# Performance work log

Hardware: AMD Instinct MI355X
Metric: run time of the kernel (lower is better)

The kernel has to match this reference:

```python
import jax, jax.numpy as jnp
import numpy as np

V, E_DIM, HID, GNN_O, HEADS = 50257, 256, 128, 128, 4
N_NODES, N_EDGES, T_LEN = 10000, 160000, 64
NEG_SLOPE = 0.2


def gatv2(x, src, dst, Wl, Wr, att, bias, concat):
    """PyG GATv2Conv (share_weights=False, self-loops already in src/dst)."""
    heads, out_ch = att.shape
    n = x.shape[0]
    xl = (x @ Wl).reshape(n, heads, out_ch)   # source transform
    xr = (x @ Wr).reshape(n, heads, out_ch)   # target transform
    e = jax.nn.leaky_relu(xl[src] + xr[dst], NEG_SLOPE)        # [E, h, c]
    logits = jnp.einsum('ehc,hc->eh', e, att)                  # [E, h]
    m = jax.ops.segment_max(logits, dst, num_segments=n)
    a = jnp.exp(logits - m[dst])
    a = a / jax.ops.segment_sum(a, dst, num_segments=n)[dst]
    out = jax.ops.segment_sum(xl[src] * a[..., None], dst, num_segments=n)
    out = out.reshape(n, heads * out_ch) if concat else out.mean(axis=1)
    return out + bias


def setup_inputs() -> dict:
    key = jax.random.key(0)
    ks = jax.random.split(key, 16)
    g = lambda k, shape: jax.random.normal(k, shape, jnp.float32) * 0.05
    x_nodes = jax.random.randint(ks[0], (N_NODES,), 0, V)
    edge_index = jax.random.randint(ks[1], (2, N_EDGES), 0, N_NODES)
    target_sequence = jax.random.randint(ks[2], (1, T_LEN), 0, V)
    return dict(
        x_nodes=x_nodes, edge_index=edge_index, target_sequence=target_sequence,
        embedding=g(ks[3], (V, E_DIM)),
        W1l=g(ks[4], (E_DIM, HEADS * HID)), W1r=g(ks[5], (E_DIM, HEADS * HID)),
        att1=g(ks[6], (HEADS, HID)), b1=jnp.zeros((HEADS * HID,), jnp.float32),
        W2l=g(ks[7], (HEADS * HID, GNN_O)), W2r=g(ks[8], (HEADS * HID, GNN_O)),
        att2=g(ks[9], (1, GNN_O)), b2=jnp.zeros((GNN_O,), jnp.float32),
        Wih=g(ks[10], (3 * HID, GNN_O + E_DIM)), Whh=g(ks[11], (3 * HID, HID)),
        bih=jnp.zeros((3 * HID,), jnp.float32), bhh=jnp.zeros((3 * HID,), jnp.float32),
        Wout=g(ks[12], (V, HID)), bout=jnp.zeros((V,), jnp.float32),
    )


def reference(x_nodes, edge_index, target_sequence, embedding,
              W1l, W1r, att1, b1, W2l, W2r, att2, b2,
              Wih, Whh, bih, bhh, Wout, bout):
    n = x_nodes.shape[0]
    loops = jnp.arange(n, dtype=edge_index.dtype)
    src = jnp.concatenate([edge_index[0], loops])   # add self-loops (PyG default)
    dst = jnp.concatenate([edge_index[1], loops])
    feats = embedding[x_nodes]                      # [N, E_DIM] (dropout off: eval)
    h1 = jax.nn.elu(gatv2(feats, src, dst, W1l, W1r, att1, b1, concat=True))
    enc = gatv2(h1, src, dst, W2l, W2r, att2, b2, concat=False)  # [N, GNN_O]
    context = enc.mean(axis=0)                      # constant across decode steps

    # teacher forcing (ratio=1.0): input tokens are SOS(0) then shifted targets
    tokens = jnp.concatenate([jnp.zeros((1,), target_sequence.dtype),
                              target_sequence[0, :-1]])

    def step(h, tok):
        x = jnp.concatenate([embedding[tok], context])          # [E_DIM+GNN_O]
        gi = Wih @ x + bih
        gh = Whh @ h + bhh
        ir, iz, inn = jnp.split(gi, 3)
        hr, hz, hn = jnp.split(gh, 3)
        r = jax.nn.sigmoid(ir + hr)
        z = jax.nn.sigmoid(iz + hz)
        cand = jnp.tanh(inn + r * hn)
        h_new = (1.0 - z) * cand + z * h
        logits = Wout @ h_new + bout
        return h_new, logits

    h0 = jnp.zeros((Whh.shape[1],), jnp.float32)
    _, logits = jax.lax.scan(step, h0, tokens)      # [T, V]
    return logits[None]                              # [1, T, V]
```

## Files before the change

### kernel.cpp

```cpp
#include <hip/hip_runtime.h>
#include <hip/hip_bf16.h>
#include <math.h>

#define NNODES 10000
#define NEDGES 160000
#define EDIM   256
#define HIDC   128
#define TLEN   64
#define VOCAB  50257
#define NEG    0.2f
#define NCTXSLOT 32

typedef __bf16 bf16x8 __attribute__((ext_vector_type(8)));
typedef float  f32x4  __attribute__((ext_vector_type(4)));

static __device__ __forceinline__ float leaky(float x){ return x > 0.f ? x : NEG*x; }
static __device__ __forceinline__ float sigm (float x){ return __fdividef(1.f, 1.f + __expf(-x)); }
static __device__ __forceinline__ float eluf (float x){ return x > 0.f ? x : expm1f(x); }
static __device__ __forceinline__ unsigned short bf16rn(float f){
  unsigned a = __float_as_uint(f);
  return (unsigned short)((a + 0x7FFFu + ((a >> 16) & 1u)) >> 16);
}
static __device__ __forceinline__ float upf(unsigned short u){ return __uint_as_float(((unsigned)u) << 16); }
static __device__ __forceinline__ float4 up4(ushort4 u){
  float4 f; f.x = upf(u.x); f.y = upf(u.y); f.z = upf(u.z); f.w = upf(u.w); return f;
}
static __device__ __forceinline__ unsigned char fp8e4m3(float f){
  return (unsigned char)(__builtin_amdgcn_cvt_pk_fp8_f32(f, f, 0, false) & 0xFF);
}
static __device__ __forceinline__ float4 up8x4(unsigned d){
  auto lo = __builtin_amdgcn_cvt_pk_f32_fp8((int)d, false);
  auto hi = __builtin_amdgcn_cvt_pk_f32_fp8((int)d, true);
  float4 f; f.x = lo[0]; f.y = lo[1]; f.z = hi[0]; f.w = hi[1]; return f;
}

#define PB_FEATS 2500
#define PB_WCAST 8783
#define PB_TR1L  8815
#define PB_TR1R  8847
#define PB_TR2L  8863
#define PB_TR2R  8879
#define PB_ZERO  8919
#define PB_AT    9047

static __device__ void tr_dev(const float* __restrict__ in, unsigned short* __restrict__ out,
                              int K, int Nin, int bx, int by, int t,
                              unsigned short (*tile)[72])
{
  int k0 = bx*64, n0 = by*64;
  int tr = t >> 4, tc4 = (t & 15)*4;
  #pragma unroll
  for (int it = 0; it < 4; ++it){
    int kr = tr + 16*it;
    float4 v = *(const float4*)(in + (size_t)(k0+kr)*Nin + n0 + tc4);
    tile[tc4+0][kr] = bf16rn(v.x);
    tile[tc4+1][kr] = bf16rn(v.y);
    tile[tc4+2][kr] = bf16rn(v.z);
    tile[tc4+3][kr] = bf16rn(v.w);
  }
  __syncthreads();
  #pragma unroll
  for (int it = 0; it < 4; ++it){
    int nr = tr + 16*it;
    ushort4 o;
    o.x = tile[nr][tc4+0]; o.y = tile[nr][tc4+1];
    o.z = tile[nr][tc4+2]; o.w = tile[nr][tc4+3];
    *(ushort4*)(out + (size_t)(n0+nr)*K + k0 + tc4) = o;
  }
}

__global__ __launch_bounds__(256) void k_prep(
    const int* __restrict__ xn, const float* __restrict__ emb,
    unsigned short* __restrict__ featsb,
    const float* __restrict__ Wout, unsigned short* __restrict__ Woutb,
    const float* __restrict__ W1l, const float* __restrict__ W1r, unsigned short* __restrict__ Bt1,
    const float* __restrict__ W2l, const float* __restrict__ W2r, unsigned short* __restrict__ Bt2,
    int* __restrict__ deg, int* __restrict__ cursor, float* __restrict__ ctxp,
    const int* __restrict__ tseq, const float* __restrict__ Wih,
    const float* __restrict__ bih, float* __restrict__ At)
{
  __shared__ unsigned short tile[64][72];
  __shared__ __align__(16) float xe[EDIM];
  int b = blockIdx.x, t = threadIdx.x;
  if (b < PB_FEATS){
    int node = b*4 + (t >> 6);
    int l = t & 63;
    float4 v = ((const float4*)(emb + (size_t)xn[node]*EDIM))[l];
    ushort4 o; o.x = bf16rn(v.x); o.y = bf16rn(v.y); o.z = bf16rn(v.z); o.w = bf16rn(v.w);
    *(ushort4*)(featsb + (size_t)node*EDIM + 4*l) = o;
  } else if (b < PB_WCAST){
    int idx = (b - PB_FEATS)*256 + t;
    if (idx < VOCAB*HIDC/4){
      float4 v = ((const float4*)Wout)[idx];
      ushort4 o; o.x = bf16rn(v.x); o.y = bf16rn(v.y); o.z = bf16rn(v.z); o.w = bf16rn(v.w);
      ((ushort4*)Woutb)[idx] = o;
    }
  } else if (b < PB_TR1L){
    int lb = b - PB_WCAST;  tr_dev(W1l, Bt1,           256, 512, lb & 3, lb >> 2, t, tile);
  } else if (b < PB_TR1R){
    int lb = b - PB_TR1L;   tr_dev(W1r, Bt1 + 512*256, 256, 512, lb & 3, lb >> 2, t, tile);
  } else if (b < PB_TR2L){
    int lb = b - PB_TR1R;   tr_dev(W2l, Bt2,           512, 128, lb & 7, lb >> 3, t, tile);
  } else if (b < PB_TR2R){
    int lb = b - PB_TR2L;   tr_dev(W2r, Bt2 + 128*512, 512, 128, lb & 7, lb >> 3, t, tile);
  } else if (b < PB_ZERO){
    int gid = (b - PB_TR2R)*256 + t;
    if (gid < NNODES){ deg[gid] = 0; cursor[gid] = 0; }
    if (gid < NCTXSLOT*HIDC) ctxp[gid] = 0.f;
  } else {
    int lb = b - PB_ZERO;
    int tt = lb >> 1;
    int row = (lb & 1)*192 + t;
    int tok = (tt == 0) ? 0 : tseq[tt-1];
    {
      if (t < 64) ((float4*)xe)[t] = ((const float4*)(emb + (size_t)tok*EDIM))[t];
      __syncthreads();
    }
    if (t < 192){
      const float4* w4 = (const float4*)(Wih + (size_t)row*384);
      const float4* x4 = (const float4*)xe;
      float a0 = 0.f, a1 = 0.f, a2 = 0.f, a3 = 0.f;
      #pragma unroll
      for (int k = 0; k < 64; k++){
        float4 w = w4[k]; float4 x = x4[k];
        a0 = fmaf(w.x, x.x, a0); a1 = fmaf(w.y, x.y, a1);
        a2 = fmaf(w.z, x.z, a2); a3 = fmaf(w.w, x.w, a3);
      }
      At[tt*384 + row] = ((a0 + a1) + (a2 + a3)) + bih[row];
    }
  }
}

__global__ void k_deg(const int* __restrict__ dst, int* __restrict__ deg){
  int e = blockIdx.x*256 + threadIdx.x;
  if (e < NEDGES) atomicAdd(&deg[dst[e]], 1);
}

__global__ __launch_bounds__(1024) void k_scan(const int* __restrict__ deg, int* __restrict__ offs){
  __shared__ int s[1024];
  int t = threadIdx.x;
  int loc[10]; int sum = 0;
  #pragma unroll
  for (int q = 0; q < 10; q++){
    int idx = t*10 + q;
    loc[q] = sum;
    sum += (idx < NNODES) ? deg[idx] : 0;
  }
  s[t] = sum;
  __syncthreads();
  for (int ofs = 1; ofs < 1024; ofs <<= 1){
    int v = (t >= ofs) ? s[t-ofs] : 0;
    __syncthreads();
    s[t] += v;
    __syncthreads();
  }
  int pre = (t > 0) ? s[t-1] : 0;
  #pragma unroll
  for (int q = 0; q < 10; q++){
    int idx = t*10 + q;
    if (idx < NNODES) offs[idx] = pre + loc[q];
  }
  if (t == 1023) offs[NNODES] = s[1023];
}

__global__ void k_scatter(const int* __restrict__ src, const int* __restrict__ dst,
                          const int* __restrict__ offs, int* __restrict__ cursor,
                          int* __restrict__ esrc){
  int e = blockIdx.x*256 + threadIdx.x;
  if (e >= NEDGES) return;
  int d = dst[e];
  int p = atomicAdd(&cursor[d], 1);
  esrc[offs[d] + p] = src[e];
}

template<int KDIM>
__global__ __launch_bounds__(256) void k_mfma(const unsigned short* __restrict__ A,
    const unsigned short* __restrict__ Bt,
    unsigned char* __restrict__ C0, unsigned short* __restrict__ C1,
    int M, int N)
{
  __shared__ __align__(16) unsigned short As[128*64];
  __shared__ __align__(16) unsigned short Bs[128*64];
  int tid = threadIdx.x;
  int l   = tid & 63;
  int wid = tid >> 6;
  int wr = wid >> 1, wc = wid & 1;
  int row0 = blockIdx.x * 128, col0 = blockIdx.y * 128;
  int lr = l & 15, kg = l >> 4;
  f32x4 acc[4][4] = {};

  for (int kt = 0; kt < KDIM/64; ++kt){
    int k0 = kt*64;
    #pragma unroll
    for (int c = 0; c < 4; ++c){
      int chunk = wid*4 + c;
      int arow = row0 + chunk*8 + (l >> 3);
      if (arow > M-1) arow = M-1;
      const unsigned short* ga = A + (size_t)arow*KDIM + k0 + (l & 7)*8;
      __builtin_amdgcn_global_load_lds(
          (const __attribute__((address_space(1))) void*)ga,
          (__attribute__((address_space(3))) void*)(As + chunk*512), 16, 0, 0);
      int brow = col0 + chunk*8 + (l >> 3);
      const unsigned short* gb = Bt + (size_t)brow*KDIM + k0 + (l & 7)*8;
      __builtin_amdgcn_global_load_lds(
          (const __attribute__((address_space(1))) void*)gb,
          (__attribute__((address_space(3))) void*)(Bs + chunk*512), 16, 0, 0);
    }
    __syncthreads();
    #pragma unroll
    for (int ks = 0; ks < 2; ++ks){
      bf16x8 af[4], bfr[4];
      #pragma unroll
      for (int m = 0; m < 4; ++m)
        af[m] = *(const bf16x8*)(As + (wr*64 + m*16 + lr)*64 + ks*32 + kg*8);
      #pragma unroll
      for (int n = 0; n < 4; ++n)
        bfr[n] = *(const bf16x8*)(Bs + (wc*64 + n*16 + lr)*64 + ks*32 + kg*8);
      #pragma unroll
      for (int m = 0; m < 4; ++m)
        #pragma unroll
        for (int n = 0; n < 4; ++n)
          acc[m][n] = __builtin_amdgcn_mfma_f32_16x16x32_bf16(af[m], bfr[n], acc[m][n], 0, 0, 0);
    }
    __syncthreads();
  }

  int half = N >> 1;
  bool isXL = (col0 < half);
  int cb = isXL ? col0 : col0 - half;
  #pragma unroll
  for (int m = 0; m < 4; ++m){
    int rbase = row0 + wr*64 + m*16 + kg*4;
    #pragma unroll
    for (int r = 0; r < 4; ++r){
      int row = rbase + r;
      if (row < M){
        #pragma unroll
        for (int n = 0; n < 4; ++n){
          int col = cb + wc*64 + n*16 + lr;
          if (isXL) C0[(size_t)row*half + col] = fp8e4m3(acc[m][n][r]);
          else      C1[(size_t)row*half + col] = bf16rn(acc[m][n][r]);
        }
      }
    }
  }
}

__global__ __launch_bounds__(256) void k_mout(const unsigned short* __restrict__ A,
    const unsigned short* __restrict__ Bt, const float* __restrict__ bias,
    float* __restrict__ out)
{
  __shared__ __align__(16) unsigned short As[64*128];
  __shared__ __align__(16) unsigned short Bs[128*128];
  int tid = threadIdx.x;
  int l   = tid & 63;
  int wid = tid >> 6;
  int col0 = blockIdx.x * 128;
  int lr = l & 15, kg = l >> 4;

  #pragma unroll
  for (int c = 0; c < 4; ++c){
    int chunk = wid*4 + c;
    const unsigned short* ga = A + (size_t)(chunk*4 + (l >> 4))*128 + (l & 15)*8;
    __builtin_amdgcn_global_load_lds(
        (const __attribute__((address_space(1))) void*)ga,
        (__attribute__((address_space(3))) void*)(As + chunk*512), 16, 0, 0);
  }
  #pragma unroll
  for (int c = 0; c < 8; ++c){
    int chunk = wid*8 + c;
    int brow = col0 + chunk*4 + (l >> 4);
    if (brow > VOCAB-1) brow = VOCAB-1;
    const unsigned short* gb = Bt + (size_t)brow*128 + (l & 15)*8;
    __builtin_amdgcn_global_load_lds(
        (const __attribute__((address_space(1))) void*)gb,
        (__attribute__((address_space(3))) void*)(Bs + chunk*512), 16, 0, 0);
  }
  __syncthreads();

  f32x4 acc[4][2] = {};
  #pragma unroll
  for (int ks = 0; ks < 4; ++ks){
    bf16x8 af[4], bfr[2];
    #pragma unroll
    for (int m = 0; m < 4; ++m)
      af[m] = *(const bf16x8*)(As + (m*16 + lr)*128 + ks*32 + kg*8);
    #pragma unroll
    for (int n = 0; n < 2; ++n)
      bfr[n] = *(const bf16x8*)(Bs + (wid*32 + n*16 + lr)*128 + ks*32 + kg*8);
    #pragma unroll
    for (int m = 0; m < 4; ++m)
      #pragma unroll
      for (int n = 0; n < 2; ++n)
        acc[m][n] = __builtin_amdgcn_mfma_f32_16x16x32_bf16(af[m], bfr[n], acc[m][n], 0, 0, 0);
  }

  #pragma unroll
  for (int n = 0; n < 2; ++n){
    int col = col0 + wid*32 + n*16 + lr;
    if (col < VOCAB){
      float bv = bias[col];
      #pragma unroll
      for (int m = 0; m < 4; ++m){
        #pragma unroll
        for (int r = 0; r < 4; ++r){
          int trow = m*16 + kg*4 + r;
          out[(size_t)trow*VOCAB + col] = acc[m][n][r] + bv;
        }
      }
    }
  }
}

__global__ __launch_bounds__(256) void k_gat1(const unsigned char* __restrict__ xl,
    const unsigned short* __restrict__ xr,
    const int* __restrict__ esrc, const int* __restrict__ offs,
    const float* __restrict__ att, const float* __restrict__ b1,
    unsigned short* __restrict__ h1b)
{
  int node = blockIdx.x*4 + (threadIdx.x >> 6);
  int l = threadIdx.x & 63;
  const unsigned short* ri = xr + (size_t)node*512;
  float4 xr1 = up4(*(const ushort4*)(ri + 4*l));
  float4 xr2 = up4(*(const ushort4*)(ri + 256 + 4*l));
  int hq = l >> 5;
  float4 at1 = *(const float4*)(att + hq*HIDC + ((4*l) & 127));
  float4 at2 = *(const float4*)(att + (2+hq)*HIDC + ((4*l) & 127));
  float4 ac1 = {0,0,0,0}, ac2 = {0,0,0,0};
  float d1 = 0.f, d2 = 0.f;
  int beg = offs[node], end = offs[node+1];
  int sB = (beg < end) ? esrc[beg] : 0;
  const unsigned char* rA = xl + (size_t)node*512;
  unsigned dA0 = *(const unsigned*)(rA + 4*l);
  unsigned dA1 = *(const unsigned*)(rA + 256 + 4*l);
  for (int p = beg-1; p < end; ++p){
    const unsigned char* rB = xl + (size_t)sB*512;
    unsigned dB0 = *(const unsigned*)(rB + 4*l);
    unsigned dB1 = *(const unsigned*)(rB + 256 + 4*l);
    int sC = (p+2 < end) ? esrc[p+2] : 0;
    float4 x1 = up8x4(dA0);
    float4 x2 = up8x4(dA1);
    float p1 = leaky(x1.x+xr1.x)*at1.x + leaky(x1.y+xr1.y)*at1.y
             + leaky(x1.z+xr1.z)*at1.z + leaky(x1.w+xr1.w)*at1.w;
    float p2 = leaky(x2.x+xr2.x)*at2.x + leaky(x2.y+xr2.y)*at2.y
             + leaky(x2.z+xr2.z)*at2.z + leaky(x2.w+xr2.w)*at2.w;
    #pragma unroll
    for (int m = 1; m <= 16; m <<= 1){
      p1 += __shfl_xor(p1, m);
      p2 += __shfl_xor(p2, m);
    }
    float w1 = __expf(p1), w2 = __expf(p2);
    ac1.x = fmaf(w1, x1.x, ac1.x); ac1.y = fmaf(w1, x1.y, ac1.y);
    ac1.z = fmaf(w1, x1.z, ac1.z); ac1.w = fmaf(w1, x1.w, ac1.w);
    ac2.x = fmaf(w2, x2.x, ac2.x); ac2.y = fmaf(w2, x2.y, ac2.y);
    ac2.z = fmaf(w2, x2.z, ac2.z); ac2.w = fmaf(w2, x2.w, ac2.w);
    d1 += w1; d2 += w2;
    dA0 = dB0; dA1 = dB1; sB = sC;
  }
  float i1 = 1.f/d1, i2 = 1.f/d2;
  const float* bq1 = b1 + 4*l;
  const float* bq2 = b1 + 256 + 4*l;
  ushort4 o1, o2;
  o1.x = bf16rn(eluf(ac1.x*i1 + bq1[0])); o1.y = bf16rn(eluf(ac1.y*i1 + bq1[1]));
  o1.z = bf16rn(eluf(ac1.z*i1 + bq1[2])); o1.w = bf16rn(eluf(ac1.w*i1 + bq1[3]));
  o2.x = bf16rn(eluf(ac2.x*i2 + bq2[0])); o2.y = bf16rn(eluf(ac2.y*i2 + bq2[1]));
  o2.z = bf16rn(eluf(ac2.z*i2 + bq2[2])); o2.w = bf16rn(eluf(ac2.w*i2 + bq2[3]));
  *(ushort4*)(h1b + (size_t)node*512 + 4*l)       = o1;
  *(ushort4*)(h1b + (size_t)node*512 + 256 + 4*l) = o2;
}

__global__ __launch_bounds__(256) void k_gat2(const unsigned char* __restrict__ xl,
    const unsigned short* __restrict__ xr,
    const int* __restrict__ esrc, const int* __restrict__ offs,
    const float* __restrict__ att2, float* __restrict__ ctxp)
{
  __shared__ float csum[128];
  int node = blockIdx.x*4 + (threadIdx.x >> 6);
  int l = threadIdx.x & 63;
  if (threadIdx.x < 128) csum[threadIdx.x] = 0.f;
  __syncthreads();
  ushort2 v = *(const ushort2*)(xr + (size_t)node*128 + 2*l);
  float2 xrv; xrv.x = upf(v.x); xrv.y = upf(v.y);
  float2 at = *(const float2*)(att2 + 2*l);
  float2 ac = {0,0}; float den = 0.f;
  int beg = offs[node], end = offs[node+1];
  int sB = (beg < end) ? esrc[beg] : 0;
  unsigned short uA = *(const unsigned short*)(xl + (size_t)node*128 + 2*l);
  for (int p = beg-1; p < end; ++p){
    unsigned short uB = *(const unsigned short*)(xl + (size_t)sB*128 + 2*l);
    int sC = (p+2 < end) ? esrc[p+2] : 0;
    auto xv = __builtin_amdgcn_cvt_pk_f32_fp8((int)(unsigned)uA, false);
    float2 x; x.x = xv[0]; x.y = xv[1];
    float pp = leaky(x.x+xrv.x)*at.x + leaky(x.y+xrv.y)*at.y;
    #pragma unroll
    for (int m = 1; m <= 32; m <<= 1) pp += __shfl_xor(pp, m);
    float w = __expf(pp);
    ac.x = fmaf(w, x.x, ac.x); ac.y = fmaf(w, x.y, ac.y);
    den += w;
    uA = uB; sB = sC;
  }
  float inv = 1.f/den;
  atomicAdd(&csum[2*l],   ac.x*inv);
  atomicAdd(&csum[2*l+1], ac.y*inv);
  __syncthreads();
  if (threadIdx.x < 128)
    atomicAdd(&ctxp[(blockIdx.x & (NCTXSLOT-1))*HIDC + threadIdx.x],
              csum[threadIdx.x] * (1.f/NNODES));
}

__global__ __launch_bounds__(384) void k_ctx(const float* __restrict__ At,
    const float* __restrict__ ctxp, const float* __restrict__ b2,
    const float* __restrict__ Wih, float* __restrict__ Gi)
{
  __shared__ alignas(16) float CTX[128];
  int tid = threadIdx.x;
  if (tid < 128){
    float s = 0.f;
    #pragma unroll
    for (int j = 0; j < NCTXSLOT; ++j) s += ctxp[j*HIDC + tid];
    CTX[tid] = s + b2[tid];
  }
  __syncthreads();
  const float4* wi = (const float4*)(Wih + (size_t)tid*384 + 256);
  const float4* c4 = (const float4*)CTX;
  float a0 = 0.f, a1 = 0.f, a2 = 0.f, a3 = 0.f;
  #pragma unroll
  for (int k = 0; k < 32; k++){
    float4 ww = wi[k]; float4 cc = c4[k];
    a0 = fmaf(ww.x, cc.x, a0); a1 = fmaf(ww.y, cc.y, a1);
    a2 = fmaf(ww.z, cc.z, a2); a3 = fmaf(ww.w, cc.w, a3);
  }
  float c = ((a0 + a1) + (a2 + a3));
  for (int t = 0; t < TLEN; t++)
    Gi[t*384 + tid] = At[t*384 + tid] + c;
}

__global__ __launch_bounds__(384) void k_gru(const float* __restrict__ Gi,
    const float* __restrict__ Whh, const float* __restrict__ bhh,
    unsigned short* __restrict__ HTt)
{
  __shared__ float GH[384];
  __shared__ alignas(16) float HS[128];
  int tid = threadIdx.x;
  float w[128];
  {
    const float4* wrow = (const float4*)(Whh + (size_t)tid*HIDC);
    #pragma unroll
    for (int k = 0; k < 32; k++){
      float4 v = wrow[k];
      w[4*k+0] = v.x; w[4*k+1] = v.y; w[4*k+2] = v.z; w[4*k+3] = v.w;
    }
  }
  float bh = bhh[tid];
  float hloc = 0.f;
  if (tid < 128) HS[tid] = 0.f;
  __syncthreads();

  const float4* H4 = (const float4*)HS;

  for (int t = 0; t < TLEN; t++){
    float gi0 = 0.f, gi1 = 0.f, gi2 = 0.f;
    if (tid < 128){
      gi0 = Gi[t*384 + tid];
      gi1 = Gi[t*384 + 128 + tid];
      gi2 = Gi[t*384 + 256 + tid];
    }
    float a0 = 0.f, a1 = 0.f, a2 = 0.f, a3 = 0.f;
    #pragma unroll
    for (int q = 0; q < 16; q++){
      float4 ha = H4[2*q];
      float4 hb = H4[2*q+1];
      a0 = fmaf(w[8*q+0], ha.x, a0);
      a1 = fmaf(w[8*q+1], ha.y, a1);
      a2 = fmaf(w[8*q+2], ha.z, a2);
      a3 = fmaf(w[8*q+3], ha.w, a3);
      a0 = fmaf(w[8*q+4], hb.x, a0);
      a1 = fmaf(w[8*q+5], hb.y, a1);
      a2 = fmaf(w[8*q+6], hb.z, a2);
      a3 = fmaf(w[8*q+7], hb.w, a3);
    }
    float acc = ((a0 + a1) + (a2 + a3)) + bh;
    if (tid >= 128) GH[tid] = acc;
    __syncthreads();
    if (tid < 128){
      float gr = gi0 + acc;
      float gz = gi1 + GH[128 + tid];
      float hn = GH[256 + tid];
      float r = sigm(gr);
      float z = sigm(gz);
      float e2 = __expf(2.f*(gi2 + r*hn));
      float cand = __fdividef(e2 - 1.f, e2 + 1.f);
      float hnew = (1.f - z)*cand + z*hloc;
      hloc = hnew;
      HS[tid] = hnew;
      HTt[t*HIDC + tid] = bf16rn(hnew);
    }
    __syncthreads();
  }
}

extern "C" void kernel_launch(void* const* d_in, const int* in_sizes, int n_in,
                              void* d_out, int out_size, void* d_ws, size_t ws_size,
                              hipStream_t stream)
{
  const int*   x_nodes = (const int*)  d_in[0];
  const int*   eidx    = (const int*)  d_in[1];
  const int*   tseq    = (const int*)  d_in[2];
  const float* emb     = (const float*)d_in[3];
  const float* W1l     = (const float*)d_in[4];
  const float* W1r     = (const float*)d_in[5];
  const float* att1    = (const float*)d_in[6];
  const float* b1      = (const float*)d_in[7];
  const float* W2l     = (const float*)d_in[8];
  const float* W2r     = (const float*)d_in[9];
  const float* att2    = (const float*)d_in[10];
  const float* b2      = (const float*)d_in[11];
  const float* Wih     = (const float*)d_in[12];
  const float* Whh     = (const float*)d_in[13];
  const float* bih     = (const float*)d_in[14];
  const float* bhh     = (const float*)d_in[15];
  const float* Wout    = (const float*)d_in[16];
  const float* bout    = (const float*)d_in[17];
  float* out = (float*)d_out;
  char*  ws  = (char*)d_ws;

  unsigned char*  xl1f8  = (unsigned char*) (ws);
  unsigned short* xr1b   = (unsigned short*)(ws + 5120000);
  unsigned short* h1b    = (unsigned short*)(ws + 15360000);
  unsigned short* featsb = (unsigned short*)(ws + 25600000);
  unsigned char*  xl2f8  = (unsigned char*) (ws + 30720000);
  unsigned short* xr2b   = (unsigned short*)(ws + 32000000);
  unsigned short* Bt1    = (unsigned short*)(ws + 34560000);
  unsigned short* Bt2    = (unsigned short*)(ws + 35084288);
  int*   deg    = (int*)(ws + 35346432);
  int*   offs   = (int*)(ws + 35386432);
  int*   cursor = (int*)(ws + 35426436);
  int*   esrc   = (int*)(ws + 35466436);
  float* At     = (float*)(ws + 36106496);
  unsigned short* HTt   = (unsigned short*)(ws + 36204800);
  unsigned short* Woutb = (unsigned short*)(ws + 36221184);
  float* ctxp   = (float*)(ws + 49086976);
  float* Gi     = (float*)(ws + 49103360);

  k_prep<<<PB_AT, 256, 0, stream>>>(x_nodes, emb, featsb, Wout, Woutb,
                                    W1l, W1r, Bt1, W2l, W2r, Bt2,
                                    deg, cursor, ctxp, tseq, Wih, bih, At);

  k_deg    <<<625, 256, 0, stream>>>(eidx + NEDGES, deg);
  k_scan   <<<1,  1024, 0, stream>>>(deg, offs);
  k_scatter<<<625, 256, 0, stream>>>(eidx, eidx + NEDGES, offs, cursor, esrc);

  k_mfma<256><<<dim3(79,8), 256, 0, stream>>>(featsb, Bt1, xl1f8, xr1b, NNODES, 1024);
  k_gat1<<<2500, 256, 0, stream>>>(xl1f8, xr1b, esrc, offs, att1, b1, h1b);

  k_mfma<512><<<dim3(79,2), 256, 0, stream>>>(h1b, Bt2, xl2f8, xr2b, NNODES, 256);
  k_gat2<<<2500, 256, 0, stream>>>(xl2f8, xr2b, esrc, offs, att2, ctxp);

  k_ctx<<<1, 384, 0, stream>>>(At, ctxp, b2, Wih, Gi);
  k_gru<<<1, 384, 0, stream>>>(Gi, Whh, bhh, HTt);

  k_mout<<<393, 256, 0, stream>>>(HTt, Woutb, bout, out);
}
```

Measured before the change: 242.1 us.

## Fuse context projection into gat2 via last-block pattern; store GRU hidden as bf16

Removes the separate single-block k_ctx launch. The last finishing k_gat2 block, found through a global atomic counter and threadfence, now reduces the context slots and computes the per-step Gi. The GRU hidden state kept in shared memory becomes bf16, which halves the LDS reads per step, with values unpacked by shifts. In exchange it adds an atomic and a fence per gat2 block, and the GRU recurrence now reads its hidden state rounded to bf16, which may drift numerically.

```diff
diff --git a/kernel.cpp b/kernel.cpp
--- a/kernel.cpp
+++ b/kernel.cpp
@@ -25,6 +25,8 @@
 static __device__ __forceinline__ float4 up4(ushort4 u){
   float4 f; f.x = upf(u.x); f.y = upf(u.y); f.z = upf(u.z); f.w = upf(u.w); return f;
 }
+static __device__ __forceinline__ float bflo(unsigned w){ return __uint_as_float(w << 16); }
+static __device__ __forceinline__ float bfhi(unsigned w){ return __uint_as_float(w & 0xFFFF0000u); }
 static __device__ __forceinline__ unsigned char fp8e4m3(float f){
   return (unsigned char)(__builtin_amdgcn_cvt_pk_fp8_f32(f, f, 0, false) & 0xFF);
 }
@@ -77,7 +79,7 @@
     const float* __restrict__ W2l, const float* __restrict__ W2r, unsigned short* __restrict__ Bt2,
     int* __restrict__ deg, int* __restrict__ cursor, float* __restrict__ ctxp,
     const int* __restrict__ tseq, const float* __restrict__ Wih,
-    const float* __restrict__ bih, float* __restrict__ At)
+    const float* __restrict__ bih, float* __restrict__ At, int* __restrict__ done)
 {
   __shared__ unsigned short tile[64][72];
   __shared__ __align__(16) float xe[EDIM];
@@ -107,6 +109,7 @@
     int gid = (b - PB_TR2R)*256 + t;
     if (gid < NNODES){ deg[gid] = 0; cursor[gid] = 0; }
     if (gid < NCTXSLOT*HIDC) ctxp[gid] = 0.f;
+    if (gid == 0) *done = 0;
   } else {
     int lb = b - PB_ZERO;
     int tt = lb >> 1;
@@ -372,7 +375,9 @@
 __global__ __launch_bounds__(256) void k_gat2(const unsigned char* __restrict__ xl,
     const unsigned short* __restrict__ xr,
     const int* __restrict__ esrc, const int* __restrict__ offs,
-    const float* __restrict__ att2, float* __restrict__ ctxp)
+    const float* __restrict__ att2, float* __restrict__ ctxp,
+    const float* __restrict__ At, const float* __restrict__ b2,
+    const float* __restrict__ Wih, float* __restrict__ Gi, int* __restrict__ done)
 {
   __shared__ float csum[128];
   int node = blockIdx.x*4 + (threadIdx.x >> 6);
@@ -406,33 +411,38 @@
   if (threadIdx.x < 128)
     atomicAdd(&ctxp[(blockIdx.x & (NCTXSLOT-1))*HIDC + threadIdx.x],
               csum[threadIdx.x] * (1.f/NNODES));
-}
-
-__global__ __launch_bounds__(384) void k_ctx(const float* __restrict__ At,
-    const float* __restrict__ ctxp, const float* __restrict__ b2,
-    const float* __restrict__ Wih, float* __restrict__ Gi)
-{
-  __shared__ alignas(16) float CTX[128];
-  int tid = threadIdx.x;
-  if (tid < 128){
+
+  __threadfence();
+  __shared__ int lastFlag;
+  if (threadIdx.x == 0)
+    lastFlag = (atomicAdd(done, 1) == (int)gridDim.x - 1);
+  __syncthreads();
+  if (!lastFlag) return;
+
+  __shared__ __align__(16) float CTX[128];
+  if (threadIdx.x < 128){
     float s = 0.f;
     #pragma unroll
-    for (int j = 0; j < NCTXSLOT; ++j) s += ctxp[j*HIDC + tid];
-    CTX[tid] = s + b2[tid];
-  }
-  __syncthreads();
-  const float4* wi = (const float4*)(Wih + (size_t)tid*384 + 256);
-  const float4* c4 = (const float4*)CTX;
-  float a0 = 0.f, a1 = 0.f, a2 = 0.f, a3 = 0.f;
-  #pragma unroll
-  for (int k = 0; k < 32; k++){
-    float4 ww = wi[k]; float4 cc = c4[k];
-    a0 = fmaf(ww.x, cc.x, a0); a1 = fmaf(ww.y, cc.y, a1);
-    a2 = fmaf(ww.z, cc.z, a2); a3 = fmaf(ww.w, cc.w, a3);
-  }
-  float c = ((a0 + a1) + (a2 + a3));
-  for (int t = 0; t < TLEN; t++)
-    Gi[t*384 + tid] = At[t*384 + tid] + c;
+    for (int j = 0; j < NCTXSLOT; ++j)
+      s += __hip_atomic_load(&ctxp[j*HIDC + threadIdx.x], __ATOMIC_RELAXED,
+                             __HIP_MEMORY_SCOPE_AGENT);
+    CTX[threadIdx.x] = s + b2[threadIdx.x];
+  }
+  __syncthreads();
+  for (int row = threadIdx.x; row < 384; row += 256){
+    const float4* wi = (const float4*)(Wih + (size_t)row*384 + 256);
+    const float4* c4 = (const float4*)CTX;
+    float a0 = 0.f, a1 = 0.f, a2 = 0.f, a3 = 0.f;
+    #pragma unroll
+    for (int k = 0; k < 32; k++){
+      float4 ww = wi[k]; float4 cc = c4[k];
+      a0 = fmaf(ww.x, cc.x, a0); a1 = fmaf(ww.y, cc.y, a1);
+      a2 = fmaf(ww.z, cc.z, a2); a3 = fmaf(ww.w, cc.w, a3);
+    }
+    float c = ((a0 + a1) + (a2 + a3));
+    for (int t = 0; t < TLEN; t++)
+      Gi[t*384 + row] = At[t*384 + row] + c;
+  }
 }
 
 __global__ __launch_bounds__(384) void k_gru(const float* __restrict__ Gi,
@@ -440,7 +450,7 @@
     unsigned short* __restrict__ HTt)
 {
   __shared__ float GH[384];
-  __shared__ alignas(16) float HS[128];
+  __shared__ alignas(16) unsigned short HSu[128];
   int tid = threadIdx.x;
   float w[128];
   {
@@ -453,10 +463,10 @@
   }
   float bh = bhh[tid];
   float hloc = 0.f;
-  if (tid < 128) HS[tid] = 0.f;
-  __syncthreads();
-
-  const float4* H4 = (const float4*)HS;
+  if (tid < 128) HSu[tid] = 0;
+  __syncthreads();
+
+  const uint4* H4 = (const uint4*)HSu;
 
   for (int t = 0; t < TLEN; t++){
     float gi0 = 0.f, gi1 = 0.f, gi2 = 0.f;
@@ -468,16 +478,15 @@
     float a0 = 0.f, a1 = 0.f, a2 = 0.f, a3 = 0.f;
     #pragma unroll
     for (int q = 0; q < 16; q++){
-      float4 ha = H4[2*q];
-      float4 hb = H4[2*q+1];
-      a0 = fmaf(w[8*q+0], ha.x, a0);
-      a1 = fmaf(w[8*q+1], ha.y, a1);
-      a2 = fmaf(w[8*q+2], ha.z, a2);
-      a3 = fmaf(w[8*q+3], ha.w, a3);
-      a0 = fmaf(w[8*q+4], hb.x, a0);
-      a1 = fmaf(w[8*q+5], hb.y, a1);
-      a2 = fmaf(w[8*q+6], hb.z, a2);
-      a3 = fmaf(w[8*q+7], hb.w, a3);
+      uint4 d = H4[q];
+      a0 = fmaf(w[8*q+0], bflo(d.x), a0);
+      a1 = fmaf(w[8*q+1], bfhi(d.x), a1);
+      a2 = fmaf(w[8*q+2], bflo(d.y), a2);
+      a3 = fmaf(w[8*q+3], bfhi(d.y), a3);
+      a0 = fmaf(w[8*q+4], bflo(d.z), a0);
+      a1 = fmaf(w[8*q+5], bfhi(d.z), a1);
+      a2 = fmaf(w[8*q+6], bflo(d.w), a2);
+      a3 = fmaf(w[8*q+7], bfhi(d.w), a3);
     }
     float acc = ((a0 + a1) + (a2 + a3)) + bh;
     if (tid >= 128) GH[tid] = acc;
@@ -492,8 +501,9 @@
       float cand = __fdividef(e2 - 1.f, e2 + 1.f);
       float hnew = (1.f - z)*cand + z*hloc;
       hloc = hnew;
-      HS[tid] = hnew;
-      HTt[t*HIDC + tid] = bf16rn(hnew);
+      unsigned short ush = bf16rn(hnew);
+      HSu[tid] = ush;
+      HTt[t*HIDC + tid] = ush;
     }
     __syncthreads();
   }
@@ -540,11 +550,12 @@
   unsigned short* HTt   = (unsigned short*)(ws + 36204800);
   unsigned short* Woutb = (unsigned short*)(ws + 36221184);
   float* ctxp   = (float*)(ws + 49086976);
-  float* Gi     = (float*)(ws + 49103360);
+  int*   done   = (int*)  (ws + 49103360);
+  float* Gi     = (float*)(ws + 49103424);
 
   k_prep<<<PB_AT, 256, 0, stream>>>(x_nodes, emb, featsb, Wout, Woutb,
                                     W1l, W1r, Bt1, W2l, W2r, Bt2,
-                                    deg, cursor, ctxp, tseq, Wih, bih, At);
+                                    deg, cursor, ctxp, tseq, Wih, bih, At, done);
 
   k_deg    <<<625, 256, 0, stream>>>(eidx + NEDGES, deg);
   k_scan   <<<1,  1024, 0, stream>>>(deg, offs);
@@ -554,9 +565,9 @@
   k_gat1<<<2500, 256, 0, stream>>>(xl1f8, xr1b, esrc, offs, att1, b1, h1b);
 
   k_mfma<512><<<dim3(79,2), 256, 0, stream>>>(h1b, Bt2, xl2f8, xr2b, NNODES, 256);
-  k_gat2<<<2500, 256, 0, stream>>>(xl2f8, xr2b, esrc, offs, att2, ctxp);
-
-  k_ctx<<<1, 384, 0, stream>>>(At, ctxp, b2, Wih, Gi);
+  k_gat2<<<2500, 256, 0, stream>>>(xl2f8, xr2b, esrc, offs, att2, ctxp,
+                                   At, b2, Wih, Gi, done);
+
   k_gru<<<1, 384, 0, stream>>>(Gi, Whh, bhh, HTt);
 
   k_mout<<<393, 256, 0, stream>>>(HTt, Woutb, bout, out);
```

Measured after the change: 435.3 us. 1.8x slower.
